# Kernel tuning notes

Measured on AMD Instinct MI355X. Metric: run time of the kernel, lower is better.

## Reference

```python
import jax, jax.numpy as jnp
import numpy as np


def setup_inputs() -> dict:
    key = jax.random.key(0)
    k1, k2 = jax.random.split(key)
    B, T, C = 32, 1024, 384
    MAX_LEN = 8192
    x = jax.random.normal(k1, (B, T, C), dtype=jnp.float32)
    duration = jax.random.randint(k2, (B, T), 0, 8, dtype=jnp.int64)
    return {"x": x, "duration": duration, "max_len": MAX_LEN}


def reference(x, duration, max_len):
    # x: [B, T, C] float; duration: [B, T] int frame counts; max_len: python int.
    # Equivalent of per-row repeat_interleave(x, duration) followed by zero-pad
    # to max_len, done as one fused cumsum + searchsorted + gather.
    B, T, C = x.shape
    cum = jnp.cumsum(duration, axis=1)            # [B, T] end frame of each phoneme
    mel_len = cum[:, -1]                          # [B] total expanded length
    pos = jnp.arange(max_len)                     # [max_len] output frame indices
    # For output frame j, source phoneme = first i with cum[i] > j
    idx = jax.vmap(lambda c: jnp.searchsorted(c, pos, side="right"))(cum)  # [B, max_len]
    idx = jnp.minimum(idx, T - 1)
    mask = pos[None, :] < mel_len[:, None]        # [B, max_len] valid (non-pad) frames
    out = jnp.take_along_axis(x, idx[:, :, None], axis=1)  # [B, max_len, C]
    out = jnp.where(mask[:, :, None], out, jnp.zeros((), dtype=x.dtype))
    return out, mel_len
```

## Files before the change

### kernel.cpp

```cpp
#include <hip/hip_runtime.h>


#define BB 32
#define TT 1024
#define CC 384
#define MAXLEN 8192
#define OUT0 (BB * MAXLEN * CC)
#define QPR (CC / 4)

typedef float f32x4 __attribute__((ext_vector_type(4)));

__global__ __launch_bounds__(256) void lr_prep(const int4* __restrict__ dur4,
                                               int* __restrict__ idx,
                                               float* __restrict__ mel_out) {
    __shared__ int cum[TT];
    __shared__ int wsum[4];
    const int b = blockIdx.x, t = threadIdx.x, lane = t & 63, w = t >> 6;

    int4 d = dur4[b * (TT / 4) + t];
    int s0 = d.x, s1 = s0 + d.y, s2 = s1 + d.z, s3 = s2 + d.w;
    int v = s3;
    #pragma unroll
    for (int dd = 1; dd < 64; dd <<= 1) {
        int u = __shfl_up(v, dd);
        if (lane >= dd) v += u;
    }
    if (lane == 63) wsum[w] = v;
    __syncthreads();
    int prefix = 0;
    #pragma unroll
    for (int i = 0; i < 4; ++i) prefix += (i < w) ? wsum[i] : 0;
    const int base = prefix + v - s3;
    cum[4 * t + 0] = base + s0;
    cum[4 * t + 1] = base + s1;
    cum[4 * t + 2] = base + s2;
    cum[4 * t + 3] = base + s3;
    __syncthreads();
    const int ml = cum[TT - 1];
    if (t == 0) mel_out[b] = (float)ml;

    #pragma unroll
    for (int k = 0; k < MAXLEN / 256; ++k) {
        int p = t + k * 256;
        int r = -1;
        if (p < ml) {
            int lo = 0, hi = TT;
            while (lo < hi) {
                int mid = (lo + hi) >> 1;
                if (cum[mid] <= p) lo = mid + 1; else hi = mid;
            }
            r = (lo < TT - 1) ? lo : (TT - 1);
        }
        idx[b * MAXLEN + p] = r;
    }
}

__global__ void lr_gather(const f32x4* __restrict__ x4,
                          const int* __restrict__ idx,
                          f32x4* __restrict__ out4) {
    const unsigned HALF = (unsigned)BB * MAXLEN * QPR / 2;
    const unsigned stride = gridDim.x * blockDim.x;
    for (unsigned q = blockIdx.x * blockDim.x + threadIdx.x; q < HALF; q += stride) {
        const unsigned q2 = q + HALF;
        unsigned row1 = q / QPR,  ln1 = q  - row1 * QPR;
        unsigned row2 = q2 / QPR, ln2 = q2 - row2 * QPR;
        int i1 = idx[row1];
        int i2 = idx[row2];
        f32x4 v1 = (f32x4)0.f, v2 = (f32x4)0.f;
        if (i1 >= 0) v1 = x4[((size_t)(row1 >> 13) * TT + (unsigned)i1) * QPR + ln1];
        if (i2 >= 0) v2 = x4[((size_t)(row2 >> 13) * TT + (unsigned)i2) * QPR + ln2];
        __builtin_nontemporal_store(v1, &out4[q]);
        __builtin_nontemporal_store(v2, &out4[q2]);
    }
}

extern "C" void kernel_launch(void* const* d_in, const int* in_sizes, int n_in,
                              void* d_out, int out_size, void* d_ws, size_t ws_size,
                              hipStream_t stream) {
    const float* x   = (const float*)d_in[0];
    const int*   dur = (const int*)d_in[1];
    float* out = (float*)d_out;

    int* idx = (int*)d_ws;

    lr_prep<<<BB, 256, 0, stream>>>((const int4*)dur, idx, out + OUT0);
    lr_gather<<<4096, 256, 0, stream>>>((const f32x4*)x, idx, (f32x4*)out);
}
```

Measured before the change: 90.37 us.

## Reorder gather work so all valid rows come first, then padding zero-fill

The gather kernel is replaced by a sweep that remaps the linear work index. All valid (non-pad) rows across batches are processed first and all padding rows after, each located by a binary search over per-batch prefix sums built in shared memory. This makes copy and zero-fill work contiguous in the thread index and avoids idx reads for pad rows. In exchange it adds per-element binary searches, a per-block prefix setup and scattered output addresses at batch boundaries, and the zero stores are no longer nontemporal.

```diff
diff --git a/kernel.cpp b/kernel.cpp
--- a/kernel.cpp
+++ b/kernel.cpp
@@ -7,11 +7,16 @@
 #define MAXLEN 8192
 #define OUT0 (BB * MAXLEN * CC)
 #define QPR (CC / 4)
+#define GBLK 4096
+#define GTHR 256
+#define STEP (GBLK * GTHR)
+#define TOTALQ (BB * MAXLEN * QPR)
 
 typedef float f32x4 __attribute__((ext_vector_type(4)));
 
 __global__ __launch_bounds__(256) void lr_prep(const int4* __restrict__ dur4,
                                                int* __restrict__ idx,
+                                               int* __restrict__ ml_out,
                                                float* __restrict__ mel_out) {
     __shared__ int cum[TT];
     __shared__ int wsum[4];
@@ -37,7 +42,7 @@
     cum[4 * t + 3] = base + s3;
     __syncthreads();
     const int ml = cum[TT - 1];
-    if (t == 0) mel_out[b] = (float)ml;
+    if (t == 0) { mel_out[b] = (float)ml; ml_out[b] = ml; }
 
     #pragma unroll
     for (int k = 0; k < MAXLEN / 256; ++k) {
@@ -55,22 +60,50 @@
     }
 }
 
-__global__ void lr_gather(const f32x4* __restrict__ x4,
-                          const int* __restrict__ idx,
-                          f32x4* __restrict__ out4) {
-    const unsigned HALF = (unsigned)BB * MAXLEN * QPR / 2;
-    const unsigned stride = gridDim.x * blockDim.x;
-    for (unsigned q = blockIdx.x * blockDim.x + threadIdx.x; q < HALF; q += stride) {
-        const unsigned q2 = q + HALF;
-        unsigned row1 = q / QPR,  ln1 = q  - row1 * QPR;
-        unsigned row2 = q2 / QPR, ln2 = q2 - row2 * QPR;
-        int i1 = idx[row1];
-        int i2 = idx[row2];
-        f32x4 v1 = (f32x4)0.f, v2 = (f32x4)0.f;
-        if (i1 >= 0) v1 = x4[((size_t)(row1 >> 13) * TT + (unsigned)i1) * QPR + ln1];
-        if (i2 >= 0) v2 = x4[((size_t)(row2 >> 13) * TT + (unsigned)i2) * QPR + ln2];
-        __builtin_nontemporal_store(v1, &out4[q]);
-        __builtin_nontemporal_store(v2, &out4[q2]);
+__global__ __launch_bounds__(GTHR) void lr_sweep(const f32x4* __restrict__ x4,
+                                                 const int* __restrict__ idx,
+                                                 const int* __restrict__ ml,
+                                                 f32x4* __restrict__ out4) {
+    __shared__ int cumL[BB + 1];
+    __shared__ int cumT[BB + 1];
+    __shared__ int mls[BB];
+    const int t = threadIdx.x;
+    if (t < BB) mls[t] = ml[t];
+    __syncthreads();
+    if (t == 0) {
+        int a = 0, c = 0;
+        cumL[0] = 0; cumT[0] = 0;
+        for (int b = 0; b < BB; ++b) {
+            a += mls[b];
+            c += MAXLEN - mls[b];
+            cumL[b + 1] = a;
+            cumT[b + 1] = c;
+        }
+    }
+    __syncthreads();
+    const int L = cumL[BB];
+
+    unsigned gid = blockIdx.x * GTHR + (unsigned)t;
+    #pragma unroll 2
+    for (unsigned g = gid; g < TOTALQ; g += STEP) {
+        unsigned r    = g / QPR;
+        unsigned lane = g - r * QPR;
+        if ((int)r < L) {
+            int lo = 0, hi = BB;
+            while (lo + 1 < hi) { int mid = (lo + hi) >> 1; if (cumL[mid] <= (int)r) lo = mid; else hi = mid; }
+            const int b = lo;
+            const int p = (int)r - cumL[b];
+            const int i = idx[b * MAXLEN + p];
+            f32x4 vv = x4[((size_t)b * TT + (unsigned)i) * QPR + lane];
+            __builtin_nontemporal_store(vv, &out4[((size_t)b * MAXLEN + p) * QPR + lane]);
+        } else {
+            const int rt = (int)r - L;
+            int lo = 0, hi = BB;
+            while (lo + 1 < hi) { int mid = (lo + hi) >> 1; if (cumT[mid] <= rt) lo = mid; else hi = mid; }
+            const int b = lo;
+            const int p = mls[b] + (rt - cumT[b]);
+            out4[((size_t)b * MAXLEN + p) * QPR + lane] = (f32x4)0.f;
+        }
     }
 }
 
@@ -82,7 +115,8 @@
     float* out = (float*)d_out;
 
     int* idx = (int*)d_ws;
+    int* ml  = idx + BB * MAXLEN;
 
-    lr_prep<<<BB, 256, 0, stream>>>((const int4*)dur, idx, out + OUT0);
-    lr_gather<<<4096, 256, 0, stream>>>((const f32x4*)x, idx, (f32x4*)out);
+    lr_prep<<<BB, 256, 0, stream>>>((const int4*)dur, idx, ml, out + OUT0);
+    lr_sweep<<<GBLK, GTHR, 0, stream>>>((const f32x4*)x, idx, ml, (f32x4*)out);
 }
```

Result: slower. 118.6 us (+31.2%).

## Compact valid rows via rowmap and split gather from zero-fill padding

Applied to the files above, without the earlier changes.

Adds a kernel that builds a compacted list of valid output rows across all batches, so the gather loop runs only over real frames, and a separate fill kernel writes zeros to pad rows. This removes the per-row index/mask branch and wasted idle work in the padded region, balancing load by total valid length. In exchange it adds two extra launches, an indirection load per element, and non-contiguous store addresses across batch boundaries. The zero writes are still required, so total bytes written stay the same.

```diff
diff --git a/kernel.cpp b/kernel.cpp
--- a/kernel.cpp
+++ b/kernel.cpp
@@ -12,6 +12,7 @@
 
 __global__ __launch_bounds__(256) void lr_prep(const int4* __restrict__ dur4,
                                                int* __restrict__ idx,
+                                               int* __restrict__ ml_out,
                                                float* __restrict__ mel_out) {
     __shared__ int cum[TT];
     __shared__ int wsum[4];
@@ -37,7 +38,7 @@
     cum[4 * t + 3] = base + s3;
     __syncthreads();
     const int ml = cum[TT - 1];
-    if (t == 0) mel_out[b] = (float)ml;
+    if (t == 0) { mel_out[b] = (float)ml; ml_out[b] = ml; }
 
     #pragma unroll
     for (int k = 0; k < MAXLEN / 256; ++k) {
@@ -55,22 +56,65 @@
     }
 }
 
-__global__ void lr_gather(const f32x4* __restrict__ x4,
-                          const int* __restrict__ idx,
-                          f32x4* __restrict__ out4) {
-    const unsigned HALF = (unsigned)BB * MAXLEN * QPR / 2;
+__global__ __launch_bounds__(256) void lr_rowmap(const int* __restrict__ ml,
+                                                 int* __restrict__ rowmap,
+                                                 int* __restrict__ totL) {
+    __shared__ int mls[BB];
+    __shared__ int base_s;
+    const int b = blockIdx.x, t = threadIdx.x;
+    if (t < BB) mls[t] = ml[t];
+    __syncthreads();
+    if (t == 0) {
+        int a = 0;
+        for (int i = 0; i < b; ++i) a += mls[i];
+        base_s = a;
+        if (b == 0) {
+            int tot = 0;
+            for (int i = 0; i < BB; ++i) tot += mls[i];
+            totL[0] = tot;
+        }
+    }
+    __syncthreads();
+    const int base = base_s, m = mls[b];
+    for (int p = t; p < m; p += 256) rowmap[base + p] = (b << 13) | p;
+}
+
+__global__ __launch_bounds__(256) void lr_gather(const f32x4* __restrict__ x4,
+                                                 const int* __restrict__ idx,
+                                                 const int* __restrict__ rowmap,
+                                                 const int* __restrict__ totLp,
+                                                 f32x4* __restrict__ out4) {
+    const unsigned totQ = (unsigned)totLp[0] * QPR;
+    const unsigned HALF = totQ >> 1;
     const unsigned stride = gridDim.x * blockDim.x;
     for (unsigned q = blockIdx.x * blockDim.x + threadIdx.x; q < HALF; q += stride) {
         const unsigned q2 = q + HALF;
-        unsigned row1 = q / QPR,  ln1 = q  - row1 * QPR;
-        unsigned row2 = q2 / QPR, ln2 = q2 - row2 * QPR;
-        int i1 = idx[row1];
-        int i2 = idx[row2];
-        f32x4 v1 = (f32x4)0.f, v2 = (f32x4)0.f;
-        if (i1 >= 0) v1 = x4[((size_t)(row1 >> 13) * TT + (unsigned)i1) * QPR + ln1];
-        if (i2 >= 0) v2 = x4[((size_t)(row2 >> 13) * TT + (unsigned)i2) * QPR + ln2];
-        __builtin_nontemporal_store(v1, &out4[q]);
-        __builtin_nontemporal_store(v2, &out4[q2]);
+        unsigned r1 = q / QPR,  ln1 = q  - r1 * QPR;
+        unsigned r2 = q2 / QPR, ln2 = q2 - r2 * QPR;
+        int rm1 = rowmap[r1];
+        int rm2 = rowmap[r2];
+        int i1 = idx[rm1];
+        int i2 = idx[rm2];
+        f32x4 v1 = x4[((size_t)(rm1 >> 13) * TT + (unsigned)i1) * QPR + ln1];
+        f32x4 v2 = x4[((size_t)(rm2 >> 13) * TT + (unsigned)i2) * QPR + ln2];
+        __builtin_nontemporal_store(v1, &out4[(size_t)rm1 * QPR + ln1]);
+        __builtin_nontemporal_store(v2, &out4[(size_t)rm2 * QPR + ln2]);
+    }
+}
+
+__global__ __launch_bounds__(256) void lr_fill(const int* __restrict__ ml,
+                                               f32x4* __restrict__ out4) {
+    const int b = blockIdx.y;
+    const int m = ml[b];
+    const int r0 = blockIdx.x * 64;
+    if (r0 + 64 <= m) return;
+    const int t = threadIdx.x;
+    f32x4* ob = out4 + (size_t)b * MAXLEN * QPR;
+    #pragma unroll 4
+    for (int k = 0; k < 64 * QPR / 256; ++k) {
+        int q = t + k * 256;
+        int row = r0 + q / QPR;
+        if (row >= m) ob[(size_t)row * QPR + (q - (q / QPR) * QPR)] = (f32x4)0.f;
     }
 }
 
@@ -81,8 +125,13 @@
     const int*   dur = (const int*)d_in[1];
     float* out = (float*)d_out;
 
-    int* idx = (int*)d_ws;
+    int* idx    = (int*)d_ws;
+    int* rowmap = idx + BB * MAXLEN;
+    int* ml     = rowmap + BB * MAXLEN;
+    int* totL   = ml + BB;
 
-    lr_prep<<<BB, 256, 0, stream>>>((const int4*)dur, idx, out + OUT0);
-    lr_gather<<<4096, 256, 0, stream>>>((const f32x4*)x, idx, (f32x4*)out);
+    lr_prep<<<BB, 256, 0, stream>>>((const int4*)dur, idx, ml, out + OUT0);
+    lr_rowmap<<<BB, 256, 0, stream>>>(ml, rowmap, totL);
+    lr_gather<<<4096, 256, 0, stream>>>((const f32x4*)x, idx, rowmap, totL, (f32x4*)out);
+    lr_fill<<<dim3(MAXLEN / 64, BB), 256, 0, stream>>>(ml, (f32x4*)out);
 }
```

After: 97.55 us. 1.08x slower.
